# Kernel optimization log

Measured on AMD Instinct MI355X. Metric: run time of the kernel, lower is better.

The kernel has to match this reference:

```python
import jax, jax.numpy as jnp
import numpy as np

B, S = 8, 1024          # sequences, tokens per sequence (batched prefill)
DIM = 2048
N_HEADS, N_KV_HEADS = 16, 8
HEAD_DIM = DIM // N_HEADS   # 128
N_REP = N_HEADS // N_KV_HEADS
BLOCK_SIZE = 16
NUM_BLOCKS = B * S // BLOCK_SIZE  # 512
T = B * S
ROPE_THETA = 10000.0


def apply_rotary_paged(x, positions):
    # x: [T, H, head_dim], positions: [T] int -- Llama-style interleaved rotary
    hd = x.shape[-1]
    inv_freq = 1.0 / (ROPE_THETA ** (jnp.arange(0, hd, 2, dtype=jnp.float32) / hd))  # [hd/2]
    ang = positions.astype(jnp.float32)[:, None] * inv_freq[None, :]                  # [T, hd/2]
    cos = jnp.cos(ang)[:, None, :]  # [T, 1, hd/2]
    sin = jnp.sin(ang)[:, None, :]
    xr, xi = x[..., 0::2], x[..., 1::2]
    out_r = xr * cos - xi * sin
    out_i = xr * sin + xi * cos
    return jnp.stack([out_r, out_i], axis=-1).reshape(x.shape).astype(x.dtype)


def setup_inputs() -> dict:
    key = jax.random.key(0)
    ks = jax.random.split(key, 6)
    std = 0.02
    x = jax.random.normal(ks[0], (T, DIM), dtype=jnp.float32)
    wq = jax.random.normal(ks[1], (DIM, N_HEADS * HEAD_DIM), dtype=jnp.float32) * std
    wk = jax.random.normal(ks[2], (DIM, N_KV_HEADS * HEAD_DIM), dtype=jnp.float32) * std
    wv = jax.random.normal(ks[3], (DIM, N_KV_HEADS * HEAD_DIM), dtype=jnp.float32) * std
    wo = jax.random.normal(ks[4], (N_HEADS * HEAD_DIM, DIM), dtype=jnp.float32) * std
    k_cache = jnp.zeros((NUM_BLOCKS, 1, N_KV_HEADS, BLOCK_SIZE, HEAD_DIM), dtype=jnp.float32)
    v_cache = jnp.zeros((NUM_BLOCKS, 1, N_KV_HEADS, BLOCK_SIZE, HEAD_DIM), dtype=jnp.float32)
    positions = jnp.tile(jnp.arange(S, dtype=jnp.int32), B)          # [T]
    tokens_per_seq = jnp.full((B,), S, dtype=jnp.int32)
    context_lengths = jnp.full((B,), S, dtype=jnp.int32)
    block_tables = jnp.arange(NUM_BLOCKS, dtype=jnp.int32).reshape(B, S // BLOCK_SIZE)
    return {"x": x, "wq": wq, "wk": wk, "wv": wv, "wo": wo,
            "k_cache": k_cache, "v_cache": v_cache,
            "positions": positions, "tokens_per_seq": tokens_per_seq,
            "context_lengths": context_lengths, "block_tables": block_tables,
            "layer_idx": 0}


def reference(x, wq, wk, wv, wo, k_cache, v_cache,
              positions, tokens_per_seq, context_lengths, block_tables, layer_idx):
    # QKV projections (Linear, no bias)
    xq = (x @ wq).reshape(T, N_HEADS, HEAD_DIM)
    xk = (x @ wk).reshape(T, N_KV_HEADS, HEAD_DIM)
    xv = (x @ wv).reshape(T, N_KV_HEADS, HEAD_DIM)
    xq = apply_rotary_paged(xq, positions)
    xk = apply_rotary_paged(xk, positions)

    # --- scatter new K/V into paged caches via block tables ---
    seq_ids = jnp.arange(T, dtype=jnp.int32) // S                 # [T]
    blk = block_tables[seq_ids, positions // BLOCK_SIZE]           # [T]
    off = positions % BLOCK_SIZE                                   # [T]
    k_cache = k_cache.at[blk, layer_idx, :, off, :].set(xk)        # [T,kvh,hd]
    v_cache = v_cache.at[blk, layer_idx, :, off, :].set(xv)

    # --- gather full K/V per sequence from the paged caches ---
    kpos = jnp.arange(S, dtype=jnp.int32)                          # [S]
    blk_g = block_tables[:, kpos // BLOCK_SIZE]                    # [B, S]
    off_g = jnp.broadcast_to(kpos % BLOCK_SIZE, (B, S))            # [B, S]
    gk = k_cache[blk_g, layer_idx, :, off_g, :]                    # [B, S, kvh, hd]
    gv = v_cache[blk_g, layer_idx, :, off_g, :]

    # GQA: repeat_interleave kv heads to n_heads
    gk = jnp.repeat(gk, N_REP, axis=2)                             # [B, S, h, hd]
    gv = jnp.repeat(gv, N_REP, axis=2)

    q = xq.reshape(B, S, N_HEADS, HEAD_DIM)
    scale = 1.0 / np.sqrt(HEAD_DIM).astype(np.float32)
    scores = jnp.einsum('bqhd,bkhd->bhqk', q, gk) * scale          # [B,h,S,S]

    # causal mask using token positions (prefill)
    q_pos = positions.reshape(B, S)
    mask = q_pos[:, None, :, None] < kpos[None, None, None, :]     # [B,1,S,S]
    scores = jnp.where(mask, -jnp.inf, scores)

    probs = jax.nn.softmax(scores.astype(jnp.float32), axis=-1).astype(q.dtype)
    attn = jnp.einsum('bhqk,bkhd->bqhd', probs, gv)                # [B,S,h,hd]
    out = attn.reshape(T, N_HEADS * HEAD_DIM) @ wo                 # resid dropout = identity (eval)
    return out
```

## Files before the change

### kernel.cpp

```cpp
#include <hip/hip_runtime.h>
#include <stdint.h>

#define TTOK  8192
#define DIMM  2048
#define NH    16
#define NKV   8
#define HD    128
#define SEQ   1024
#define BATCH 8
#define BLKSZ 16

typedef unsigned short u16;
typedef __attribute__((ext_vector_type(8))) short bfrag;
typedef __attribute__((ext_vector_type(4))) float f32x4;

__device__ __forceinline__ float bf2f(u16 u) {
  unsigned int v = ((unsigned int)u) << 16;
  float f; __builtin_memcpy(&f, &v, 4); return f;
}
__device__ __forceinline__ u16 f2bf(float f) {
  unsigned int v; __builtin_memcpy(&v, &f, 4);
  v = v + 0x7FFFu + ((v >> 16) & 1u);
  return (u16)(v >> 16);
}

__device__ __forceinline__ void gll16(const void* g, void* l) {
  __builtin_amdgcn_global_load_lds(
      (__attribute__((address_space(1))) void*)(g),
      (__attribute__((address_space(3))) void*)(l), 16, 0, 0);
}
__device__ __forceinline__ void hard_fence() {
  asm volatile("" ::: "memory");
  __builtin_amdgcn_s_waitcnt(0);
  asm volatile("" ::: "memory");
}

__global__ __launch_bounds__(256) void f32_to_bf16(const float* __restrict__ in,
                                                   u16* __restrict__ out, size_t n) {
  size_t i = ((size_t)blockIdx.x * 256 + threadIdx.x) * 8;
  if (i >= n) return;
  float4 a = *(const float4*)(in + i);
  float4 b = *(const float4*)(in + i + 4);
  union { u16 o[8]; uint4 v; } u;
  u.o[0] = f2bf(a.x); u.o[1] = f2bf(a.y); u.o[2] = f2bf(a.z); u.o[3] = f2bf(a.w);
  u.o[4] = f2bf(b.x); u.o[5] = f2bf(b.y); u.o[6] = f2bf(b.z); u.o[7] = f2bf(b.w);
  *(uint4*)(out + i) = u.v;
}

__global__ __launch_bounds__(256) void ktranspose_f(const float* __restrict__ in,
                                                    u16* __restrict__ out, int K, int N) {
  __shared__ __align__(16) u16 tile[64 * 65];
  int n0 = blockIdx.x * 64, k0 = blockIdx.y * 64;
  int tx = threadIdx.x & 63, ty = threadIdx.x >> 6;
  for (int r = 0; r < 16; ++r) {
    int kk = r * 4 + ty;
    tile[kk * 65 + tx] = f2bf(in[(size_t)(k0 + kk) * N + n0 + tx]);
  }
  __syncthreads();
  for (int r = 0; r < 16; ++r) {
    int nn = r * 4 + ty;
    out[(size_t)(n0 + nn) * K + k0 + tx] = tile[tx * 65 + nn];
  }
}

template <typename OutT>
__global__ __launch_bounds__(256) void gemm_bt(const u16* __restrict__ A,
                                               const u16* __restrict__ Bt,
                                               OutT* __restrict__ C,
                                               int M, int N, int K) {
  __shared__ __align__(16) u16 As[128 * 32];
  __shared__ __align__(16) u16 Bs[128 * 32];
  int tid = threadIdx.x;
  int wave = tid >> 6, lane = tid & 63, quad = lane >> 4, l15 = lane & 15;
  int m0 = blockIdx.y * 128, n0 = blockIdx.x * 128;
  int wm = (wave >> 1) * 64, wn = (wave & 1) * 64;

  f32x4 acc[4][4];
  for (int i = 0; i < 4; ++i)
    for (int j = 0; j < 4; ++j) acc[i][j] = (f32x4){0.f, 0.f, 0.f, 0.f};

  int g0 = wave * 64 + lane;
  int g1 = 256 + wave * 64 + lane;
  const u16* Arow0 = A + (size_t)(m0 + (g0 >> 2)) * K + (g0 & 3) * 8;
  const u16* Arow1 = A + (size_t)(m0 + (g1 >> 2)) * K + (g1 & 3) * 8;
  const u16* Brow0 = Bt + (size_t)(n0 + (g0 >> 2)) * K + (g0 & 3) * 8;
  const u16* Brow1 = Bt + (size_t)(n0 + (g1 >> 2)) * K + (g1 & 3) * 8;
  char* AsB = (char*)As;
  char* BsB = (char*)Bs;
  int lds0 = wave * 1024, lds1 = 4096 + wave * 1024;

  for (int k0 = 0; k0 < K; k0 += 32) {
    __syncthreads();
    asm volatile("" ::: "memory");
    gll16(Arow0 + k0, AsB + lds0);
    gll16(Arow1 + k0, AsB + lds1);
    gll16(Brow0 + k0, BsB + lds0);
    gll16(Brow1 + k0, BsB + lds1);
    hard_fence();
    __syncthreads();

    bfrag af[4], bfv[4];
    for (int im = 0; im < 4; ++im) {
      int m = wm + im * 16 + l15;
      af[im] = *(const bfrag*)(AsB + m * 64 + quad * 16);
    }
    for (int jn = 0; jn < 4; ++jn) {
      int n = wn + jn * 16 + l15;
      bfv[jn] = *(const bfrag*)(BsB + n * 64 + quad * 16);
    }
    for (int im = 0; im < 4; ++im)
      for (int jn = 0; jn < 4; ++jn)
        acc[im][jn] = __builtin_amdgcn_mfma_f32_16x16x32_bf16(af[im], bfv[jn], acc[im][jn], 0, 0, 0);
  }

  for (int im = 0; im < 4; ++im)
    for (int jn = 0; jn < 4; ++jn)
      for (int r = 0; r < 4; ++r) {
        int row = m0 + wm + im * 16 + quad * 4 + r;
        int col = n0 + wn + jn * 16 + l15;
        if constexpr (__is_same(OutT, float))
          C[(size_t)row * N + col] = acc[im][jn][r];
        else
          C[(size_t)row * N + col] = f2bf(acc[im][jn][r]);
      }
}

__global__ __launch_bounds__(256) void rope_scatter(const u16* __restrict__ xqkv,
                                                    const int* __restrict__ positions,
                                                    const int* __restrict__ btab,
                                                    u16* __restrict__ qb,
                                                    u16* __restrict__ kb,
                                                    u16* __restrict__ vbuf) {
  int t = blockIdx.x;
  int tid = threadIdx.x;
  int b = t >> 10, srow = t & 1023;
  int pos = positions[t];
  int blk = btab[b * (SEQ / BLKSZ) + (pos >> 4)];
  int off = pos & (BLKSZ - 1);
  int c0 = tid * 16;

  struct __align__(16) { uint4 a, bq; } vv, oo;
  const u16* src = xqkv + (size_t)t * 4096 + c0;
  vv.a  = *(const uint4*)src;
  vv.bq = *(const uint4*)(src + 8);
  const u16* v = (const u16*)&vv;
  u16* o = (u16*)&oo;

  if (c0 < 3072) {
    int dbase = c0 & 127;
    float fpos = (float)pos;
    for (int j = 0; j < 8; ++j) {
      int i = (dbase >> 1) + j;
      float inv = exp2f(-(float)i * (13.287712379549449f / 64.0f));
      float ang = fpos * inv;
      float sn, cs;
      sincosf(ang, &sn, &cs);
      float fr = bf2f(v[2 * j]), fi = bf2f(v[2 * j + 1]);
      o[2 * j]     = f2bf(fr * cs - fi * sn);
      o[2 * j + 1] = f2bf(fr * sn + fi * cs);
    }
  } else {
    for (int j = 0; j < 16; ++j) o[j] = v[j];
  }

  u16* dst;
  if (c0 < 2048) {
    int head = c0 >> 7, d0 = c0 & 127;
    dst = qb + (((size_t)(b * NH + head)) * SEQ + srow) * HD + d0;
  } else if (c0 < 3072) {
    int cc = c0 - 2048;
    int kvh = cc >> 7, d0 = cc & 127;
    dst = kb + (((size_t)(blk * NKV + kvh) * BLKSZ + off)) * HD + d0;
  } else {
    int cc = c0 - 3072;
    int kvh = cc >> 7, d0 = cc & 127;
    dst = vbuf + (((size_t)(blk * NKV + kvh) * BLKSZ + off)) * HD + d0;
  }
  *(uint4*)dst = oo.a;
  *(uint4*)(dst + 8) = oo.bq;
}

#define KS_STRIDE 272
#define VT_STRIDE 80
#define PS_STRIDE 80

__global__ __launch_bounds__(512) void attn_kernel(const u16* __restrict__ Q,
                                                   const u16* __restrict__ Kc,
                                                   const u16* __restrict__ Vc,
                                                   const int* __restrict__ positions,
                                                   const int* __restrict__ btab,
                                                   u16* __restrict__ O) {
  __shared__ __align__(16) u16 Ks[32 * (KS_STRIDE / 2)];
  __shared__ __align__(16) u16 Vt[128 * (VT_STRIDE / 2)];
  __shared__ __align__(16) u16 Ps[8 * 16 * (PS_STRIDE / 2)];
  const float SM_SCALE = 0.08838834764831845f;
  const float LOG2E    = 1.4426950408889634f;
  const float NEGBIG   = -30000.0f;
  const float DEFER_THR = 8.0f;

  int tid = threadIdx.x;
  int wave = tid >> 6, lane = tid & 63, quad = lane >> 4, l15 = lane & 15;
  int bid = blockIdx.x;
  int bh = bid >> 2, pr = bid & 3;
  int b = bh >> 4, h = bh & 15, kvh = h >> 1;
  const int* btrow = btab + b * (SEQ / BLKSZ);

  char* KsB = (char*)Ks;
  char* VtB = (char*)Vt;
  char* myPsB = (char*)Ps + wave * 16 * PS_STRIDE;

  int tokp = (tid & 15) * 2;
  int vd0 = (tid >> 4) * 4;

  for (int pass = 0; pass < 2; ++pass) {
    int yt = pass ? (7 - pr) : pr;
    int q0 = yt * 128;
    int qw = q0 + wave * 16;

    const u16* Qbase = Q + ((size_t)bh * SEQ + qw) * HD;

    bfrag aq[4];
#pragma unroll
    for (int kb2 = 0; kb2 < 4; ++kb2)
      aq[kb2] = *(const bfrag*)(Qbase + (size_t)l15 * HD + kb2 * 32 + quad * 8);

    int qpos[4];
#pragma unroll
    for (int r = 0; r < 4; ++r)
      qpos[r] = positions[(size_t)b * SEQ + qw + quad * 4 + r];

    f32x4 oa[8];
#pragma unroll
    for (int jd = 0; jd < 8; ++jd) oa[jd] = (f32x4){0.f, 0.f, 0.f, 0.f};
    float m_i[4], l_i[4];
#pragma unroll
    for (int r = 0; r < 4; ++r) { m_i[r] = NEGBIG; l_i[r] = 0.f; }

    int kend = q0 + 128;
    for (int kt = 0; kt < kend; kt += 32) {
      int blkA = btrow[(kt >> 4)], blkB = btrow[(kt >> 4) + 1];
      const u16* KbA = Kc + ((size_t)(blkA * NKV + kvh) * BLKSZ) * HD;
      const u16* KbB = Kc + ((size_t)(blkB * NKV + kvh) * BLKSZ) * HD;
      const u16* VbA = Vc + ((size_t)(blkA * NKV + kvh) * BLKSZ) * HD;
      const u16* VbB = Vc + ((size_t)(blkB * NKV + kvh) * BLKSZ) * HD;

      __syncthreads();
      {
        int row = tid >> 4, dg = tid & 15;
        const u16* kb_src = (row < 16) ? (KbA + (size_t)row * HD)
                                       : (KbB + (size_t)(row - 16) * HD);
        *(uint4*)(KsB + row * KS_STRIDE + dg * 16) = *(const uint4*)(kb_src + dg * 8);
      }
      {
        const u16* vb_src = (tokp < 16) ? (VbA + (size_t)tokp * HD)
                                        : (VbB + (size_t)(tokp - 16) * HD);
        uint2 r0 = *(const uint2*)(vb_src + vd0);
        uint2 r1 = *(const uint2*)(vb_src + HD + vd0);
        const u16* p0 = (const u16*)&r0;
        const u16* p1 = (const u16*)&r1;
#pragma unroll
        for (int jj = 0; jj < 4; ++jj) {
          int d = vd0 + jj;
          unsigned int val = (unsigned int)p0[jj] | ((unsigned int)p1[jj] << 16);
          *(unsigned int*)(VtB + d * VT_STRIDE + tokp * 2) = val;
        }
      }
      __syncthreads();

      if (kt <= qw + 15) {
        f32x4 sa0 = (f32x4){0.f, 0.f, 0.f, 0.f};
        f32x4 sa1 = (f32x4){0.f, 0.f, 0.f, 0.f};
#pragma unroll
        for (int kb2 = 0; kb2 < 4; ++kb2) {
          bfrag bk0 = *(const bfrag*)(KsB + l15 * KS_STRIDE + (kb2 * 4 + quad) * 16);
          bfrag bk1 = *(const bfrag*)(KsB + (16 + l15) * KS_STRIDE + (kb2 * 4 + quad) * 16);
          sa0 = __builtin_amdgcn_mfma_f32_16x16x32_bf16(aq[kb2], bk0, sa0, 0, 0, 0);
          sa1 = __builtin_amdgcn_mfma_f32_16x16x32_bf16(aq[kb2], bk1, sa1, 0, 0, 0);
        }

        float s0v[4], s1v[4], mx[4];
#pragma unroll
        for (int r = 0; r < 4; ++r) {
          float s0 = sa0[r] * SM_SCALE;
          float s1 = sa1[r] * SM_SCALE;
          if (kt + l15 > qpos[r]) s0 = NEGBIG;
          if (kt + 16 + l15 > qpos[r]) s1 = NEGBIG;
          float m = fmaxf(s0, s1);
          m = fmaxf(m, __shfl_xor(m, 1, 64));
          m = fmaxf(m, __shfl_xor(m, 2, 64));
          m = fmaxf(m, __shfl_xor(m, 4, 64));
          m = fmaxf(m, __shfl_xor(m, 8, 64));
          s0v[r] = s0; s1v[r] = s1; mx[r] = m;
        }

        float pr0[4], pr1[4];
        bool ok = (mx[0] <= m_i[0] + DEFER_THR) && (mx[1] <= m_i[1] + DEFER_THR) &&
                  (mx[2] <= m_i[2] + DEFER_THR) && (mx[3] <= m_i[3] + DEFER_THR);
        if (__all(ok)) {
#pragma unroll
          for (int r = 0; r < 4; ++r) {
            float p0 = exp2f((s0v[r] - m_i[r]) * LOG2E);
            float p1 = exp2f((s1v[r] - m_i[r]) * LOG2E);
            float rs = p0 + p1;
            rs += __shfl_xor(rs, 1, 64);
            rs += __shfl_xor(rs, 2, 64);
            rs += __shfl_xor(rs, 4, 64);
            rs += __shfl_xor(rs, 8, 64);
            l_i[r] += rs;
            pr0[r] = p0; pr1[r] = p1;
          }
        } else {
          float alpha[4];
#pragma unroll
          for (int r = 0; r < 4; ++r) {
            float mnew = fmaxf(m_i[r], mx[r]);
            float al = exp2f((m_i[r] - mnew) * LOG2E);
            float p0 = exp2f((s0v[r] - mnew) * LOG2E);
            float p1 = exp2f((s1v[r] - mnew) * LOG2E);
            float rs = p0 + p1;
            rs += __shfl_xor(rs, 1, 64);
            rs += __shfl_xor(rs, 2, 64);
            rs += __shfl_xor(rs, 4, 64);
            rs += __shfl_xor(rs, 8, 64);
            l_i[r] = l_i[r] * al + rs;
            m_i[r] = mnew;
            alpha[r] = al;
            pr0[r] = p0; pr1[r] = p1;
          }
#pragma unroll
          for (int jd = 0; jd < 8; ++jd) {
            oa[jd][0] *= alpha[0];
            oa[jd][1] *= alpha[1];
            oa[jd][2] *= alpha[2];
            oa[jd][3] *= alpha[3];
          }
        }

#pragma unroll
        for (int r = 0; r < 4; ++r) {
          int q = quad * 4 + r;
          *(u16*)(myPsB + q * PS_STRIDE + l15 * 2)        = f2bf(pr0[r]);
          *(u16*)(myPsB + q * PS_STRIDE + (16 + l15) * 2) = f2bf(pr1[r]);
        }
        bfrag ap = *(const bfrag*)(myPsB + l15 * PS_STRIDE + quad * 16);
#pragma unroll
        for (int jd = 0; jd < 8; ++jd) {
          int d = jd * 16 + l15;
          bfrag bv = *(const bfrag*)(VtB + d * VT_STRIDE + quad * 16);
          oa[jd] = __builtin_amdgcn_mfma_f32_16x16x32_bf16(ap, bv, oa[jd], 0, 0, 0);
        }
      }
    }

#pragma unroll
    for (int r = 0; r < 4; ++r) {
      float inv = 1.0f / fmaxf(l_i[r], 1e-30f);
      size_t trow = (size_t)b * SEQ + qw + quad * 4 + r;
#pragma unroll
      for (int jd = 0; jd < 8; ++jd)
        O[trow * 2048 + (size_t)h * HD + jd * 16 + l15] = f2bf(oa[jd][r] * inv);
    }
  }
}

extern "C" void kernel_launch(void* const* d_in, const int* in_sizes, int n_in,
                              void* d_out, int out_size, void* d_ws, size_t ws_size,
                              hipStream_t stream) {
  (void)in_sizes; (void)n_in; (void)out_size;
  const float* xf  = (const float*)d_in[0];
  const float* wqf = (const float*)d_in[1];
  const float* wkf = (const float*)d_in[2];
  const float* wvf = (const float*)d_in[3];
  const float* wof = (const float*)d_in[4];
  const int* positions = (const int*)d_in[7];
  const int* btab      = (const int*)d_in[10];
  float* out = (float*)d_out;

  u16* ws    = (u16*)d_ws;
  u16* woT   = ws;
  u16* wqkvT = woT + (size_t)2048 * 2048;
  u16* xbf   = wqkvT + (size_t)4096 * 2048;
  u16* xqkv  = xbf + (size_t)8192 * 2048;
  u16* qb    = xqkv + (size_t)8192 * 4096;
  u16* kbuf  = qb + (size_t)8192 * 2048;
  u16* vbuf  = kbuf + (size_t)8192 * 1024;
  u16* wsend = vbuf + (size_t)8192 * 1024;

  size_t base_elems = (size_t)(wsend - ws);
  size_t obuf_elems = (size_t)8192 * 2048;
  u16* obuf;
  if (ws_size >= (base_elems + obuf_elems) * sizeof(u16))
    obuf = wsend;
  else
    obuf = wqkvT;

  if (ws_size < base_elems * sizeof(u16)) return;

  f32_to_bf16<<<dim3(8192), 256, 0, stream>>>(xf, xbf, (size_t)8192 * 2048);
  ktranspose_f<<<dim3(32, 32), 256, 0, stream>>>(wqf, wqkvT, 2048, 2048);
  ktranspose_f<<<dim3(16, 32), 256, 0, stream>>>(wkf, wqkvT + (size_t)2048 * 2048, 2048, 1024);
  ktranspose_f<<<dim3(16, 32), 256, 0, stream>>>(wvf, wqkvT + (size_t)3072 * 2048, 2048, 1024);
  ktranspose_f<<<dim3(32, 32), 256, 0, stream>>>(wof, woT, 2048, 2048);
  gemm_bt<u16><<<dim3(32, 64), 256, 0, stream>>>(xbf, wqkvT, xqkv, 8192, 4096, 2048);
  rope_scatter<<<dim3(8192), 256, 0, stream>>>(xqkv, positions, btab, qb, kbuf, vbuf);
  attn_kernel<<<dim3(512), 512, 0, stream>>>(qb, kbuf, vbuf, positions, btab, obuf);
  gemm_bt<float><<<dim3(16, 64), 256, 0, stream>>>(obuf, woT, out, 8192, 2048, 2048);
}
```

Measured before the change: 663.4 us.

## Double KV tile to 64 tokens with register prefetch and folded exp2 scaling

Enlarges each attention KV tile from 32 to 64 tokens, halving the number of block barriers per query tile. The next tile's K and V are loaded into registers right after the barrier, so global loads overlap the MFMA and softmax work. The softmax scale and log2e are folded into one multiply per score so max and running sums stay in the exp2 domain. In exchange it uses more registers and LDS per block, under a new launch-bounds occupancy hint, and masked waves now sync on larger, partly wasted tiles near the diagonal.

Result: slower. 747.6 us (+12.7%).

```diff
diff --git a/kernel.cpp b/kernel.cpp
--- a/kernel.cpp
+++ b/kernel.cpp
@@ -180,23 +180,26 @@
   *(uint4*)(dst + 8) = oo.bq;
 }
 
+#define KVT 64
 #define KS_STRIDE 272
-#define VT_STRIDE 80
-#define PS_STRIDE 80
-
-__global__ __launch_bounds__(512) void attn_kernel(const u16* __restrict__ Q,
-                                                   const u16* __restrict__ Kc,
-                                                   const u16* __restrict__ Vc,
-                                                   const int* __restrict__ positions,
-                                                   const int* __restrict__ btab,
-                                                   u16* __restrict__ O) {
-  __shared__ __align__(16) u16 Ks[32 * (KS_STRIDE / 2)];
-  __shared__ __align__(16) u16 Vt[128 * (VT_STRIDE / 2)];
+#define VT_STRIDE 144
+#define PS_STRIDE 144
+
+__global__ __launch_bounds__(512, 4) void attn_kernel(const u16* __restrict__ Q,
+                                                      const u16* __restrict__ Kc,
+                                                      const u16* __restrict__ Vc,
+                                                      const int* __restrict__ positions,
+                                                      const int* __restrict__ btab,
+                                                      u16* __restrict__ O) {
+  __shared__ __align__(16) u16 Ks[KVT * (KS_STRIDE / 2)];
+  __shared__ __align__(16) u16 Vt[HD * (VT_STRIDE / 2)];
   __shared__ __align__(16) u16 Ps[8 * 16 * (PS_STRIDE / 2)];
   const float SM_SCALE = 0.08838834764831845f;
   const float LOG2E    = 1.4426950408889634f;
+  const float C1       = SM_SCALE * LOG2E;
   const float NEGBIG   = -30000.0f;
-  const float DEFER_THR = 8.0f;
+  const float NEGINIT  = -1e30f;
+  const float DEFER2   = 8.0f * LOG2E;
 
   int tid = threadIdx.x;
   int wave = tid >> 6, lane = tid & 63, quad = lane >> 4, l15 = lane & 15;
@@ -209,8 +212,26 @@
   char* VtB = (char*)Vt;
   char* myPsB = (char*)Ps + wave * 16 * PS_STRIDE;
 
-  int tokp = (tid & 15) * 2;
-  int vd0 = (tid >> 4) * 4;
+  int tokA = tid >> 4;
+  int tokB = tokA + 32;
+  int dgK  = tid & 15;
+  int tokV = (tid & 31) * 2;
+  int vd0  = (tid >> 5) * 8;
+
+  uint4 kr0, kr1, vr0, vr1;
+
+  auto load_tile = [&](int kti) {
+    int i0 = kti >> 4;
+    int b0 = btrow[i0], b1 = btrow[i0 + 1], b2 = btrow[i0 + 2], b3 = btrow[i0 + 3];
+    const u16* KA = Kc + ((size_t)(((tokA < 16) ? b0 : b1) * NKV + kvh) * BLKSZ + (tokA & 15)) * HD + dgK * 8;
+    const u16* KB = Kc + ((size_t)(((tokB < 48) ? b2 : b3) * NKV + kvh) * BLKSZ + (tokB & 15)) * HD + dgK * 8;
+    kr0 = *(const uint4*)KA;
+    kr1 = *(const uint4*)KB;
+    int bv = (tokV < 16) ? b0 : (tokV < 32) ? b1 : (tokV < 48) ? b2 : b3;
+    const u16* VA = Vc + ((size_t)(bv * NKV + kvh) * BLKSZ + (tokV & 15)) * HD + vd0;
+    vr0 = *(const uint4*)VA;
+    vr1 = *(const uint4*)(VA + HD);
+  };
 
   for (int pass = 0; pass < 2; ++pass) {
     int yt = pass ? (7 - pr) : pr;
@@ -232,100 +253,99 @@
     f32x4 oa[8];
 #pragma unroll
     for (int jd = 0; jd < 8; ++jd) oa[jd] = (f32x4){0.f, 0.f, 0.f, 0.f};
-    float m_i[4], l_i[4];
-#pragma unroll
-    for (int r = 0; r < 4; ++r) { m_i[r] = NEGBIG; l_i[r] = 0.f; }
+    float m2_i[4], l_i[4];
+#pragma unroll
+    for (int r = 0; r < 4; ++r) { m2_i[r] = NEGINIT; l_i[r] = 0.f; }
 
     int kend = q0 + 128;
-    for (int kt = 0; kt < kend; kt += 32) {
-      int blkA = btrow[(kt >> 4)], blkB = btrow[(kt >> 4) + 1];
-      const u16* KbA = Kc + ((size_t)(blkA * NKV + kvh) * BLKSZ) * HD;
-      const u16* KbB = Kc + ((size_t)(blkB * NKV + kvh) * BLKSZ) * HD;
-      const u16* VbA = Vc + ((size_t)(blkA * NKV + kvh) * BLKSZ) * HD;
-      const u16* VbB = Vc + ((size_t)(blkB * NKV + kvh) * BLKSZ) * HD;
-
+    load_tile(0);
+
+    for (int kt = 0; kt < kend; kt += KVT) {
       __syncthreads();
+      *(uint4*)(KsB + tokA * KS_STRIDE + dgK * 16) = kr0;
+      *(uint4*)(KsB + tokB * KS_STRIDE + dgK * 16) = kr1;
       {
-        int row = tid >> 4, dg = tid & 15;
-        const u16* kb_src = (row < 16) ? (KbA + (size_t)row * HD)
-                                       : (KbB + (size_t)(row - 16) * HD);
-        *(uint4*)(KsB + row * KS_STRIDE + dg * 16) = *(const uint4*)(kb_src + dg * 8);
-      }
-      {
-        const u16* vb_src = (tokp < 16) ? (VbA + (size_t)tokp * HD)
-                                        : (VbB + (size_t)(tokp - 16) * HD);
-        uint2 r0 = *(const uint2*)(vb_src + vd0);
-        uint2 r1 = *(const uint2*)(vb_src + HD + vd0);
-        const u16* p0 = (const u16*)&r0;
-        const u16* p1 = (const u16*)&r1;
-#pragma unroll
-        for (int jj = 0; jj < 4; ++jj) {
-          int d = vd0 + jj;
+        const u16* p0 = (const u16*)&vr0;
+        const u16* p1 = (const u16*)&vr1;
+#pragma unroll
+        for (int jj = 0; jj < 8; ++jj) {
           unsigned int val = (unsigned int)p0[jj] | ((unsigned int)p1[jj] << 16);
-          *(unsigned int*)(VtB + d * VT_STRIDE + tokp * 2) = val;
+          *(unsigned int*)(VtB + (vd0 + jj) * VT_STRIDE + tokV * 2) = val;
         }
       }
       __syncthreads();
 
+      if (kt + KVT < kend) load_tile(kt + KVT);
+
       if (kt <= qw + 15) {
-        f32x4 sa0 = (f32x4){0.f, 0.f, 0.f, 0.f};
-        f32x4 sa1 = (f32x4){0.f, 0.f, 0.f, 0.f};
+        f32x4 sa[4];
+#pragma unroll
+        for (int jn = 0; jn < 4; ++jn) sa[jn] = (f32x4){0.f, 0.f, 0.f, 0.f};
 #pragma unroll
         for (int kb2 = 0; kb2 < 4; ++kb2) {
-          bfrag bk0 = *(const bfrag*)(KsB + l15 * KS_STRIDE + (kb2 * 4 + quad) * 16);
-          bfrag bk1 = *(const bfrag*)(KsB + (16 + l15) * KS_STRIDE + (kb2 * 4 + quad) * 16);
-          sa0 = __builtin_amdgcn_mfma_f32_16x16x32_bf16(aq[kb2], bk0, sa0, 0, 0, 0);
-          sa1 = __builtin_amdgcn_mfma_f32_16x16x32_bf16(aq[kb2], bk1, sa1, 0, 0, 0);
-        }
-
-        float s0v[4], s1v[4], mx[4];
+#pragma unroll
+          for (int jn = 0; jn < 4; ++jn) {
+            bfrag bk = *(const bfrag*)(KsB + (jn * 16 + l15) * KS_STRIDE + (kb2 * 4 + quad) * 16);
+            sa[jn] = __builtin_amdgcn_mfma_f32_16x16x32_bf16(aq[kb2], bk, sa[jn], 0, 0, 0);
+          }
+        }
+
+        float z[4][4];
+        float m2x[4];
 #pragma unroll
         for (int r = 0; r < 4; ++r) {
-          float s0 = sa0[r] * SM_SCALE;
-          float s1 = sa1[r] * SM_SCALE;
-          if (kt + l15 > qpos[r]) s0 = NEGBIG;
-          if (kt + 16 + l15 > qpos[r]) s1 = NEGBIG;
-          float m = fmaxf(s0, s1);
-          m = fmaxf(m, __shfl_xor(m, 1, 64));
-          m = fmaxf(m, __shfl_xor(m, 2, 64));
-          m = fmaxf(m, __shfl_xor(m, 4, 64));
-          m = fmaxf(m, __shfl_xor(m, 8, 64));
-          s0v[r] = s0; s1v[r] = s1; mx[r] = m;
-        }
-
-        float pr0[4], pr1[4];
-        bool ok = (mx[0] <= m_i[0] + DEFER_THR) && (mx[1] <= m_i[1] + DEFER_THR) &&
-                  (mx[2] <= m_i[2] + DEFER_THR) && (mx[3] <= m_i[3] + DEFER_THR);
+#pragma unroll
+          for (int jn = 0; jn < 4; ++jn) {
+            float s = sa[jn][r];
+            if (kt + jn * 16 + l15 > qpos[r]) s = NEGBIG;
+            z[jn][r] = s;
+          }
+          float m0 = fmaxf(fmaxf(z[0][r], z[1][r]), fmaxf(z[2][r], z[3][r]));
+          m0 = fmaxf(m0, __shfl_xor(m0, 1, 64));
+          m0 = fmaxf(m0, __shfl_xor(m0, 2, 64));
+          m0 = fmaxf(m0, __shfl_xor(m0, 4, 64));
+          m0 = fmaxf(m0, __shfl_xor(m0, 8, 64));
+          m2x[r] = m0 * C1;
+        }
+
+        bool ok = (m2x[0] <= m2_i[0] + DEFER2) && (m2x[1] <= m2_i[1] + DEFER2) &&
+                  (m2x[2] <= m2_i[2] + DEFER2) && (m2x[3] <= m2_i[3] + DEFER2);
         if (__all(ok)) {
 #pragma unroll
           for (int r = 0; r < 4; ++r) {
-            float p0 = exp2f((s0v[r] - m_i[r]) * LOG2E);
-            float p1 = exp2f((s1v[r] - m_i[r]) * LOG2E);
-            float rs = p0 + p1;
+            float rs = 0.f;
+#pragma unroll
+            for (int jn = 0; jn < 4; ++jn) {
+              float pv = exp2f(z[jn][r] * C1 - m2_i[r]);
+              z[jn][r] = pv;
+              rs += pv;
+            }
             rs += __shfl_xor(rs, 1, 64);
             rs += __shfl_xor(rs, 2, 64);
             rs += __shfl_xor(rs, 4, 64);
             rs += __shfl_xor(rs, 8, 64);
             l_i[r] += rs;
-            pr0[r] = p0; pr1[r] = p1;
           }
         } else {
           float alpha[4];
 #pragma unroll
           for (int r = 0; r < 4; ++r) {
-            float mnew = fmaxf(m_i[r], mx[r]);
-            float al = exp2f((m_i[r] - mnew) * LOG2E);
-            float p0 = exp2f((s0v[r] - mnew) * LOG2E);
-            float p1 = exp2f((s1v[r] - mnew) * LOG2E);
-            float rs = p0 + p1;
+            float m2n = fmaxf(m2_i[r], m2x[r]);
+            float al = exp2f(m2_i[r] - m2n);
+            float rs = 0.f;
+#pragma unroll
+            for (int jn = 0; jn < 4; ++jn) {
+              float pv = exp2f(z[jn][r] * C1 - m2n);
+              z[jn][r] = pv;
+              rs += pv;
+            }
             rs += __shfl_xor(rs, 1, 64);
             rs += __shfl_xor(rs, 2, 64);
             rs += __shfl_xor(rs, 4, 64);
             rs += __shfl_xor(rs, 8, 64);
             l_i[r] = l_i[r] * al + rs;
-            m_i[r] = mnew;
+            m2_i[r] = m2n;
             alpha[r] = al;
-            pr0[r] = p0; pr1[r] = p1;
           }
 #pragma unroll
           for (int jd = 0; jd < 8; ++jd) {
@@ -339,15 +359,19 @@
 #pragma unroll
         for (int r = 0; r < 4; ++r) {
           int q = quad * 4 + r;
-          *(u16*)(myPsB + q * PS_STRIDE + l15 * 2)        = f2bf(pr0[r]);
-          *(u16*)(myPsB + q * PS_STRIDE + (16 + l15) * 2) = f2bf(pr1[r]);
-        }
-        bfrag ap = *(const bfrag*)(myPsB + l15 * PS_STRIDE + quad * 16);
+#pragma unroll
+          for (int jn = 0; jn < 4; ++jn)
+            *(u16*)(myPsB + q * PS_STRIDE + (jn * 16 + l15) * 2) = f2bf(z[jn][r]);
+        }
+        bfrag ap0 = *(const bfrag*)(myPsB + l15 * PS_STRIDE + quad * 16);
+        bfrag ap1 = *(const bfrag*)(myPsB + l15 * PS_STRIDE + 64 + quad * 16);
 #pragma unroll
         for (int jd = 0; jd < 8; ++jd) {
           int d = jd * 16 + l15;
-          bfrag bv = *(const bfrag*)(VtB + d * VT_STRIDE + quad * 16);
-          oa[jd] = __builtin_amdgcn_mfma_f32_16x16x32_bf16(ap, bv, oa[jd], 0, 0, 0);
+          bfrag bv0 = *(const bfrag*)(VtB + d * VT_STRIDE + quad * 16);
+          bfrag bv1 = *(const bfrag*)(VtB + d * VT_STRIDE + 64 + quad * 16);
+          oa[jd] = __builtin_amdgcn_mfma_f32_16x16x32_bf16(ap0, bv0, oa[jd], 0, 0, 0);
+          oa[jd] = __builtin_amdgcn_mfma_f32_16x16x32_bf16(ap1, bv1, oa[jd], 0, 0, 0);
         }
       }
     }
```
